# Performance work log

Hardware: AMD Instinct MI355X
Metric: run time of the kernel (lower is better)

## Reference

```python
import jax, jax.numpy as jnp
import numpy as np

B, N, F_IN, DEG = 8, 4096, 8, 8
E = B * N * DEG
MAX_RADIUS, NUM_BASIS, HIDDEN = 3.0, 10, 64
MUL0, MUL1 = 32, 16  # irreps_potential = '32x0e + 16x1o'
W_NUMEL = F_IN * (MUL0 + MUL1)  # 384


def setup_inputs() -> dict:
    key = jax.random.key(0)
    k1, k2, k3, k4, k5, k6 = jax.random.split(key, 6)
    node_features = jax.random.normal(k1, (B, N, F_IN), jnp.float32)
    pos = 4.0 * jax.random.uniform(k2, (B, N, 3), dtype=jnp.float32)  # box so many pairs fall inside max_radius
    # static-shape stand-in for radius_graph: DEG random neighbors per node, within each graph, no self loops
    src = jax.random.randint(k3, (B, N * DEG), 0, N)
    off = jax.random.randint(k4, (B, N * DEG), 1, N)
    dst = (src + off) % N
    boff = (jnp.arange(B) * N)[:, None]
    edge_src = (src + boff).reshape(-1).astype(jnp.int32)
    edge_dst = (dst + boff).reshape(-1).astype(jnp.int32)
    W1 = jax.random.normal(k5, (NUM_BASIS, HIDDEN), jnp.float32)
    W2 = jax.random.normal(k6, (HIDDEN, W_NUMEL), jnp.float32)
    return {"node_features": node_features, "pos": pos, "edge_src": edge_src,
            "edge_dst": edge_dst, "W1": W1, "W2": W2}


def _forward(node_features, pos, edge_src, edge_dst, W1, W2):
    pos_flat = pos.reshape(-1, 3)            # [B*N, 3]
    x_flat = node_features.reshape(-1, F_IN)  # [B*N, F_IN]
    edge_vec = pos_flat[edge_src] - pos_flat[edge_dst]  # [E,3]
    r = jnp.sqrt(jnp.sum(edge_vec * edge_vec, axis=1) + 1e-18)  # [E]

    # soft_one_hot_linspace(r, 0, R, num_basis, basis='smooth_finite', cutoff=True) * sqrt(num_basis)
    values = jnp.linspace(0.0, MAX_RADIUS, NUM_BASIS + 2)[1:-1]
    step = values[1] - values[0]
    d = (r[:, None] - values[None, :]) / step
    inside = jnp.abs(d) < 1.0
    y = jnp.where(inside, jnp.maximum(1.0 - d * d, 1e-7), 1.0)
    emb = jnp.where(inside, 1.14136 * jnp.exp(2.0) * jnp.exp(-1.0 / y), 0.0)
    emb = emb * (NUM_BASIS ** 0.5)           # [E, num_basis]

    # soft_unit_step(10 * (1 - r/R))
    t = 10.0 * (1.0 - r / MAX_RADIUS)
    w_cut = jnp.where(t > 0.0, jnp.exp(-1.0 / jnp.where(t > 0.0, t, 1.0)), 0.0)

    # spherical harmonics lmax=2, normalize=True, 'component' normalization
    u = edge_vec / r[:, None]
    ux, uy, uz = u[:, 0], u[:, 1], u[:, 2]
    sh1 = jnp.sqrt(3.0) * u                  # l=1 (component norm); sh0 == 1
    c15 = np.sqrt(15.0)
    sh2 = jnp.stack([c15 * ux * uy, c15 * uy * uz, 0.5 * np.sqrt(5.0) * (3 * uz * uz - 1.0),
                     c15 * ux * uz, 0.5 * c15 * (ux * ux - uy * uy)], axis=1)
    del sh2  # 2e couples 0e input only to 2e, which is absent from '32x0e+16x1o' -> no path

    # FullyConnectedNet([num_basis, hidden, weight_numel], silu) -> per-edge TP weights
    h = jax.nn.silu(emb @ (W1 / np.sqrt(NUM_BASIS)))
    w = h @ (W2 / np.sqrt(HIDDEN))           # [E, 384]
    wA = w[:, : F_IN * MUL0].reshape(-1, F_IN, MUL0)
    wB = w[:, F_IN * MUL0:].reshape(-1, F_IN, MUL1)

    # FullyConnectedTensorProduct (uvw), shared_weights=False, path norm 1/sqrt(fan_in)
    x_src = x_flat[edge_src]                 # gather [E, F_IN]
    inv = 1.0 / np.sqrt(F_IN)
    out0 = jnp.einsum('eu,euw->ew', x_src, wA) * inv            # 0e x 0e -> 32x0e
    out1 = jnp.einsum('eu,ei,euw->ewi', x_src, sh1, wB) * inv   # 0e x 1o -> 16x1o
    potential = jnp.concatenate([out0, out1.reshape(-1, 3 * MUL1)], axis=1)  # [E, 80]

    # scatter-add to destination nodes
    nodes = jax.ops.segment_sum(w_cut[:, None] * potential, edge_dst, num_segments=B * N)
    psi = nodes[:, :3].reshape(B, N, 3)
    curl = jnp.stack([psi[..., 2] - psi[..., 1],
                      psi[..., 0] - psi[..., 2],
                      psi[..., 1] - psi[..., 0]], axis=-1)       # [B, N, 3]
    return curl


def reference(node_features, pos, edge_src, edge_dst, W1, W2):
    return _forward(node_features, pos, edge_src, edge_dst, W1, W2)
```

## Files before the change

### kernel.cpp

```cpp
#include <hip/hip_runtime.h>
#include <hip/hip_fp16.h>


#define THREADS 256
#define RTAB 2048
#define ROWH 32

__global__ __launch_bounds__(THREADS) void se3_build_table(
    const float* __restrict__ W1,
    const float* __restrict__ W2,
    __half* __restrict__ T,
    float4* __restrict__ zbuf,
    int zcount4)
{
    __shared__ float sW1[10 * 65];
    __shared__ float sW2[64][25];

    for (int t = threadIdx.x; t < 640; t += THREADS) {
        int j = t >> 6, k = t & 63;
        sW1[j * 65 + k] = W1[t];
    }
    for (int t = threadIdx.x; t < 64 * 24; t += THREADS) {
        int k = t / 24, j = t - 24 * k;
        int u = j / 3, c = j - 3 * u;
        sW2[k][j] = W2[k * 384 + u * 32 + c];
    }

    int g = blockIdx.x * THREADS + threadIdx.x;

    float4 z = make_float4(0.f, 0.f, 0.f, 0.f);
    for (int idx = g; idx < zcount4; idx += gridDim.x * THREADS)
        zbuf[idx] = z;

    __syncthreads();

    if (g >= RTAB * 8) return;
    int i = g >> 3;
    int u = g & 7;

    float r = 3.0f * (float)i / (float)(RTAB - 1);
    float q0 = 0.f, q1 = 0.f;
    float t10 = 10.0f - (10.0f / 3.0f) * r;
    if (t10 > 0.0f) {
        const float C0 = 8.43357306907549f;
        float q  = r * (11.0f / 3.0f);
        int   jf = (int)q;
        float da = q - (float)jf;
        float db = da - 1.0f;
        float ya = fmaxf(1.0f - da * da, 1e-7f);
        float yb = fmaxf(1.0f - db * db, 1e-7f);
        int ja = jf - 1, jb = jf;
        float ea = (ja >= 0) ? C0 * __expf(-1.0f / ya) : 0.0f;
        float eb = (jb <= 9) ? C0 * __expf(-1.0f / yb) : 0.0f;
        int jac = ja < 0 ? 0 : ja;
        int jbc = jb > 9 ? 9 : jb;
        const float* w1a = sW1 + jac * 65;
        const float* w1b = sW1 + jbc * 65;

        float a0 = 0.f, a1 = 0.f, a2 = 0.f;
#pragma unroll 8
        for (int k = 0; k < 64; ++k) {
            float pre = ea * w1a[k] + eb * w1b[k];
            float h   = pre * __builtin_amdgcn_rcpf(1.0f + __expf(-pre));
            a0 = fmaf(h, sW2[k][u * 3 + 0], a0);
            a1 = fmaf(h, sW2[k][u * 3 + 1], a1);
            a2 = fmaf(h, sW2[k][u * 3 + 2], a2);
        }
        float sc = __expf(-1.0f / t10) * 0.04419417382415922f;
        q0 = (a2 - a1) * sc;
        q1 = (a0 - a2) * sc;
    }

    __half h0 = __float2half(q0);
    __half h1 = __float2half(q1);
    size_t base = (size_t)i * ROWH + 4 * u;
    T[base + 0] = h0;
    T[base + 2] = h1;
    if (i > 0) {
        T[base - ROWH + 1] = h0;
        T[base - ROWH + 3] = h1;
    }
    if (i == RTAB - 1) {
        T[base + 1] = h0;
        T[base + 3] = h1;
    }
}

__global__ __launch_bounds__(THREADS) void se3_edge_kernel(
    const float* __restrict__ x,
    const float* __restrict__ pos,
    const int*   __restrict__ esrc,
    const int*   __restrict__ edst,
    const __half* __restrict__ T,
    float*       __restrict__ outbuf,
    int E, int ncopies, int outN2)
{
    int e = blockIdx.x * THREADS + threadIdx.x;
    if (e >= E) return;

    int s = esrc[e];
    int d = edst[e];

    float ex = pos[3 * s + 0] - pos[3 * d + 0];
    float ey = pos[3 * s + 1] - pos[3 * d + 1];
    float ez = pos[3 * s + 2] - pos[3 * d + 2];
    float r  = sqrtf(ex * ex + ey * ey + ez * ez + 1e-18f);

    if (r >= 3.0f) return;

    float tq = r * ((float)(RTAB - 1) / 3.0f);
    int   i  = (int)tq;
    if (i > RTAB - 2) i = RTAB - 2;
    float f  = tq - (float)i;

    const float4* rowp = reinterpret_cast<const float4*>(T + (size_t)i * ROWH);
    const float4* xf   = reinterpret_cast<const float4*>(x + 8 * (size_t)s);
    float4 r0 = rowp[0], r1 = rowp[1], r2 = rowp[2], r3 = rowp[3];
    float4 xA = xf[0];
    float4 xB = xf[1];
    float x0 = xA.x, x1 = xA.y, x2 = xA.z, x3 = xA.w;
    float x4 = xB.x, x5 = xB.y, x6 = xB.z, x7 = xB.w;

    float c0 = 0.f, c1 = 0.f;
    auto proc = [&](float4 v, float xu, float xv) {
        union { float4 f4; __half2 h[4]; } cv; cv.f4 = v;
        float2 a0 = __half22float2(cv.h[0]);
        float2 a1 = __half22float2(cv.h[1]);
        float2 a2 = __half22float2(cv.h[2]);
        float2 a3 = __half22float2(cv.h[3]);
        c0 = fmaf(xu, fmaf(f, a0.y - a0.x, a0.x), c0);
        c1 = fmaf(xu, fmaf(f, a1.y - a1.x, a1.x), c1);
        c0 = fmaf(xv, fmaf(f, a2.y - a2.x, a2.x), c0);
        c1 = fmaf(xv, fmaf(f, a3.y - a3.x, a3.x), c1);
    };
    proc(r0, x0, x1);
    proc(r1, x2, x3);
    proc(r2, x4, x5);
    proc(r3, x6, x7);

    float* ob = outbuf + (size_t)(blockIdx.x % ncopies) * outN2 + 2 * d;
    unsafeAtomicAdd(ob + 0, c0);
    unsafeAtomicAdd(ob + 1, c1);
}

__global__ __launch_bounds__(THREADS) void se3_reduce_kernel(
    const float* __restrict__ ws, float* __restrict__ out,
    int nNodes, int ncopies, int outN2)
{
    int n = blockIdx.x * THREADS + threadIdx.x;
    if (n >= nNodes) return;
    const float2* w = reinterpret_cast<const float2*>(ws);
    int stride2 = outN2 >> 1;
    float a = 0.f, b = 0.f;
    for (int c = 0; c < ncopies; ++c) {
        float2 v = w[(size_t)c * stride2 + n];
        a += v.x; b += v.y;
    }
    out[3 * n + 0] = a;
    out[3 * n + 1] = b;
    out[3 * n + 2] = -a - b;
}

extern "C" void kernel_launch(void* const* d_in, const int* in_sizes, int n_in,
                              void* d_out, int out_size, void* d_ws, size_t ws_size,
                              hipStream_t stream) {
    const float* x    = (const float*)d_in[0];
    const float* pos  = (const float*)d_in[1];
    const int*   esrc = (const int*)d_in[2];
    const int*   edst = (const int*)d_in[3];
    const float* W1   = (const float*)d_in[4];
    const float* W2   = (const float*)d_in[5];
    float* out = (float*)d_out;

    int E      = in_sizes[2];
    int outN   = out_size;
    int nNodes = outN / 3;
    int outN2  = 2 * nNodes;

    size_t tableBytes = (size_t)RTAB * ROWH * sizeof(__half);
    __half* T      = (__half*)d_ws;
    float*  copies = (float*)((char*)d_ws + tableBytes);

    size_t copyBytes = (size_t)outN2 * sizeof(float);
    int ncopies = 1;
    if (ws_size > tableBytes + copyBytes) {
        size_t rem = ws_size - tableBytes;
        int nc = (int)(rem / copyBytes);
        if (nc > 8) nc = 8;
        if (nc < 1) nc = 1;
        ncopies = nc;
    }
    int zcount4 = (int)(((size_t)ncopies * outN2) / 4);

    se3_build_table<<<(RTAB * 8) / THREADS, THREADS, 0, stream>>>(
        W1, W2, T, (float4*)copies, zcount4);

    se3_edge_kernel<<<(E + THREADS - 1) / THREADS, THREADS, 0, stream>>>(
        x, pos, esrc, edst, T, copies, E, ncopies, outN2);

    se3_reduce_kernel<<<(nNodes + THREADS - 1) / THREADS, THREADS, 0, stream>>>(
        copies, out, nNodes, ncopies, outN2);
}
```

Baseline: 95.78 us.

## Fuse table build and edge scatter into one cooperative kernel with grid sync

Replaces the three launches (table build with zeroing, edge scatter into replicated buffers, reduction) with a single cooperative kernel. It zeroes the output, builds the lookup table, does a grid-wide sync, then runs a grid-stride edge loop that atomically adds all three curl components straight into the output. The W2 differences are also precomputed in shared memory, so the table loop needs two FMAs per step instead of three. This removes launch overhead and the reduce pass, at the cost of a grid barrier, more atomics per edge (three instead of two) and contention on a single output copy. There are also host-side occupancy queries on every call.

New measurement: 218.0 us. 128% more time.

```diff
diff --git a/kernel.cpp b/kernel.cpp
--- a/kernel.cpp
+++ b/kernel.cpp
@@ -1,40 +1,34 @@
 #include <hip/hip_runtime.h>
 #include <hip/hip_fp16.h>
+#include <hip/hip_cooperative_groups.h>
+
+namespace cg = cooperative_groups;
 
 
 #define THREADS 256
 #define RTAB 2048
 #define ROWH 32
-
-__global__ __launch_bounds__(THREADS) void se3_build_table(
-    const float* __restrict__ W1,
-    const float* __restrict__ W2,
-    __half* __restrict__ T,
-    float4* __restrict__ zbuf,
-    int zcount4)
-{
-    __shared__ float sW1[10 * 65];
-    __shared__ float sW2[64][25];
-
+#define TBLOCKS ((RTAB * 8) / THREADS)
+
+
+__device__ __forceinline__ void stage_weights(const float* __restrict__ W1,
+                                              const float* __restrict__ W2,
+                                              float* sW1, float* sDW2) {
     for (int t = threadIdx.x; t < 640; t += THREADS) {
         int j = t >> 6, k = t & 63;
         sW1[j * 65 + k] = W1[t];
     }
-    for (int t = threadIdx.x; t < 64 * 24; t += THREADS) {
-        int k = t / 24, j = t - 24 * k;
-        int u = j / 3, c = j - 3 * u;
-        sW2[k][j] = W2[k * 384 + u * 32 + c];
-    }
-
-    int g = blockIdx.x * THREADS + threadIdx.x;
-
-    float4 z = make_float4(0.f, 0.f, 0.f, 0.f);
-    for (int idx = g; idx < zcount4; idx += gridDim.x * THREADS)
-        zbuf[idx] = z;
-
-    __syncthreads();
-
-    if (g >= RTAB * 8) return;
+    for (int t = threadIdx.x; t < 64 * 16; t += THREADS) {
+        int k = t >> 4, j = t & 15;
+        int u = j >> 1;
+        const float* w2 = W2 + k * 384 + u * 32;
+        sDW2[t] = (j & 1) ? (w2[0] - w2[2]) : (w2[2] - w2[1]);
+    }
+}
+
+__device__ __forceinline__ void table_entry(int g, const float* sW1,
+                                            const float* sDW2,
+                                            __half* __restrict__ T) {
     int i = g >> 3;
     int u = g & 7;
 
@@ -56,19 +50,19 @@
         int jbc = jb > 9 ? 9 : jb;
         const float* w1a = sW1 + jac * 65;
         const float* w1b = sW1 + jbc * 65;
-
-        float a0 = 0.f, a1 = 0.f, a2 = 0.f;
+        const float* dw  = sDW2 + 2 * u;
+
+        float a0 = 0.f, a1 = 0.f;
 #pragma unroll 8
         for (int k = 0; k < 64; ++k) {
             float pre = ea * w1a[k] + eb * w1b[k];
             float h   = pre * __builtin_amdgcn_rcpf(1.0f + __expf(-pre));
-            a0 = fmaf(h, sW2[k][u * 3 + 0], a0);
-            a1 = fmaf(h, sW2[k][u * 3 + 1], a1);
-            a2 = fmaf(h, sW2[k][u * 3 + 2], a2);
+            a0 = fmaf(h, dw[16 * k + 0], a0);
+            a1 = fmaf(h, dw[16 * k + 1], a1);
         }
         float sc = __expf(-1.0f / t10) * 0.04419417382415922f;
-        q0 = (a2 - a1) * sc;
-        q1 = (a0 - a2) * sc;
+        q0 = a0 * sc;
+        q1 = a1 * sc;
     }
 
     __half h0 = __float2half(q0);
@@ -86,18 +80,11 @@
     }
 }
 
-__global__ __launch_bounds__(THREADS) void se3_edge_kernel(
-    const float* __restrict__ x,
-    const float* __restrict__ pos,
-    const int*   __restrict__ esrc,
-    const int*   __restrict__ edst,
-    const __half* __restrict__ T,
-    float*       __restrict__ outbuf,
-    int E, int ncopies, int outN2)
-{
-    int e = blockIdx.x * THREADS + threadIdx.x;
-    if (e >= E) return;
-
+__device__ __forceinline__ void edge_work(int e,
+    const float* __restrict__ x, const float* __restrict__ pos,
+    const int* __restrict__ esrc, const int* __restrict__ edst,
+    const __half* __restrict__ T, float* __restrict__ out)
+{
     int s = esrc[e];
     int d = edst[e];
 
@@ -118,8 +105,6 @@
     float4 r0 = rowp[0], r1 = rowp[1], r2 = rowp[2], r3 = rowp[3];
     float4 xA = xf[0];
     float4 xB = xf[1];
-    float x0 = xA.x, x1 = xA.y, x2 = xA.z, x3 = xA.w;
-    float x4 = xB.x, x5 = xB.y, x6 = xB.z, x7 = xB.w;
 
     float c0 = 0.f, c1 = 0.f;
     auto proc = [&](float4 v, float xu, float xv) {
@@ -133,33 +118,73 @@
         c0 = fmaf(xv, fmaf(f, a2.y - a2.x, a2.x), c0);
         c1 = fmaf(xv, fmaf(f, a3.y - a3.x, a3.x), c1);
     };
-    proc(r0, x0, x1);
-    proc(r1, x2, x3);
-    proc(r2, x4, x5);
-    proc(r3, x6, x7);
-
-    float* ob = outbuf + (size_t)(blockIdx.x % ncopies) * outN2 + 2 * d;
+    proc(r0, xA.x, xA.y);
+    proc(r1, xA.z, xA.w);
+    proc(r2, xB.x, xB.y);
+    proc(r3, xB.z, xB.w);
+
+    float* ob = out + 3 * (size_t)d;
     unsafeAtomicAdd(ob + 0, c0);
     unsafeAtomicAdd(ob + 1, c1);
-}
-
-__global__ __launch_bounds__(THREADS) void se3_reduce_kernel(
-    const float* __restrict__ ws, float* __restrict__ out,
-    int nNodes, int ncopies, int outN2)
-{
-    int n = blockIdx.x * THREADS + threadIdx.x;
-    if (n >= nNodes) return;
-    const float2* w = reinterpret_cast<const float2*>(ws);
-    int stride2 = outN2 >> 1;
-    float a = 0.f, b = 0.f;
-    for (int c = 0; c < ncopies; ++c) {
-        float2 v = w[(size_t)c * stride2 + n];
-        a += v.x; b += v.y;
-    }
-    out[3 * n + 0] = a;
-    out[3 * n + 1] = b;
-    out[3 * n + 2] = -a - b;
-}
+    unsafeAtomicAdd(ob + 2, -c0 - c1);
+}
+
+
+__global__ __launch_bounds__(THREADS) void se3_fused(
+    const float* __restrict__ x, const float* __restrict__ pos,
+    const int* __restrict__ esrc, const int* __restrict__ edst,
+    const float* __restrict__ W1, const float* __restrict__ W2,
+    __half* __restrict__ T, float* __restrict__ out, int E, int outN)
+{
+    __shared__ float sW1[10 * 65];
+    __shared__ float sDW2[64 * 16];
+
+    int tid = blockIdx.x * THREADS + threadIdx.x;
+    int nth = gridDim.x * THREADS;
+
+    float4 z = make_float4(0.f, 0.f, 0.f, 0.f);
+    for (int idx = tid; idx < (outN >> 2); idx += nth)
+        reinterpret_cast<float4*>(out)[idx] = z;
+
+    if (blockIdx.x < TBLOCKS) {
+        stage_weights(W1, W2, sW1, sDW2);
+        __syncthreads();
+        table_entry(tid, sW1, sDW2, T);
+    }
+
+    cg::this_grid().sync();
+
+    for (int e = tid; e < E; e += nth)
+        edge_work(e, x, pos, esrc, edst, T, out);
+}
+
+
+__global__ __launch_bounds__(THREADS) void se3_build_split(
+    const float* __restrict__ W1, const float* __restrict__ W2,
+    __half* __restrict__ T, float4* __restrict__ zbuf, int zcount4)
+{
+    __shared__ float sW1[10 * 65];
+    __shared__ float sDW2[64 * 16];
+
+    int g = blockIdx.x * THREADS + threadIdx.x;
+    float4 z = make_float4(0.f, 0.f, 0.f, 0.f);
+    for (int idx = g; idx < zcount4; idx += gridDim.x * THREADS)
+        zbuf[idx] = z;
+
+    stage_weights(W1, W2, sW1, sDW2);
+    __syncthreads();
+    if (g < RTAB * 8) table_entry(g, sW1, sDW2, T);
+}
+
+__global__ __launch_bounds__(THREADS) void se3_edge_split(
+    const float* __restrict__ x, const float* __restrict__ pos,
+    const int* __restrict__ esrc, const int* __restrict__ edst,
+    const __half* __restrict__ T, float* __restrict__ out, int E)
+{
+    int e = blockIdx.x * THREADS + threadIdx.x;
+    if (e < E) edge_work(e, x, pos, esrc, edst, T, out);
+}
+
 
 extern "C" void kernel_launch(void* const* d_in, const int* in_sizes, int n_in,
                               void* d_out, int out_size, void* d_ws, size_t ws_size,
@@ -172,32 +197,38 @@
     const float* W2   = (const float*)d_in[5];
     float* out = (float*)d_out;
 
-    int E      = in_sizes[2];
-    int outN   = out_size;
-    int nNodes = outN / 3;
-    int outN2  = 2 * nNodes;
-
-    size_t tableBytes = (size_t)RTAB * ROWH * sizeof(__half);
-    __half* T      = (__half*)d_ws;
-    float*  copies = (float*)((char*)d_ws + tableBytes);
-
-    size_t copyBytes = (size_t)outN2 * sizeof(float);
-    int ncopies = 1;
-    if (ws_size > tableBytes + copyBytes) {
-        size_t rem = ws_size - tableBytes;
-        int nc = (int)(rem / copyBytes);
-        if (nc > 8) nc = 8;
-        if (nc < 1) nc = 1;
-        ncopies = nc;
-    }
-    int zcount4 = (int)(((size_t)ncopies * outN2) / 4);
-
-    se3_build_table<<<(RTAB * 8) / THREADS, THREADS, 0, stream>>>(
-        W1, W2, T, (float4*)copies, zcount4);
-
-    se3_edge_kernel<<<(E + THREADS - 1) / THREADS, THREADS, 0, stream>>>(
-        x, pos, esrc, edst, T, copies, E, ncopies, outN2);
-
-    se3_reduce_kernel<<<(nNodes + THREADS - 1) / THREADS, THREADS, 0, stream>>>(
-        copies, out, nNodes, ncopies, outN2);
-}
+    int E    = in_sizes[2];
+    int outN = out_size;
+    __half* T = (__half*)d_ws;
+
+    int blocksPerCU = 0;
+    if (hipOccupancyMaxActiveBlocksPerMultiprocessor(
+            &blocksPerCU, se3_fused, THREADS, 0) != hipSuccess || blocksPerCU < 1)
+        blocksPerCU = 2;
+    int nCU = 0;
+    int dev = 0;
+    (void)hipGetDevice(&dev);
+    if (hipDeviceGetAttribute(&nCU, hipDeviceAttributeMultiprocessorCount, dev)
+            != hipSuccess || nCU < 1)
+        nCU = 256;
+
+    long cap  = (long)blocksPerCU * (long)nCU;
+    int  grid = (E + THREADS - 1) / THREADS;
+    if ((long)grid > cap) grid = (int)cap;
+    if (grid < TBLOCKS) grid = TBLOCKS;
+
+    void* args[] = {(void*)&x, (void*)&pos, (void*)&esrc, (void*)&edst,
+                    (void*)&W1, (void*)&W2, (void*)&T, (void*)&out,
+                    (void*)&E, (void*)&outN};
+
+    hipError_t err = hipLaunchCooperativeKernel(
+        se3_fused, dim3(grid), dim3(THREADS), args, 0, stream);
+
+    if (err != hipSuccess) {
+        (void)hipGetLastError();
+        se3_build_split<<<TBLOCKS, THREADS, 0, stream>>>(
+            W1, W2, T, (float4*)out, outN / 4);
+        se3_edge_split<<<(E + THREADS - 1) / THREADS, THREADS, 0, stream>>>(
+            x, pos, esrc, edst, T, out, E);
+    }
+}
```

## Repack positions to float4, precompute W2 differences, raise atomic copy count

Applied to the files above, without the earlier changes.

The table-build kernel now also repacks node positions into a padded float4 array so the edge kernel fetches each endpoint with one vector load instead of three scalar gathers. The W2 column differences used for the curl are folded into shared memory ahead of the hidden-unit loop, which cuts one accumulator per thread. The number of atomic-target copies may now go up to sixteen, spreading contention at the cost of more zeroing and reduction traffic, and the build kernel runs on a larger grid to cover the repack and zero passes.

After: 96.48 us. Within noise of the previous version (+0.7%).

```diff
diff --git a/kernel.cpp b/kernel.cpp
--- a/kernel.cpp
+++ b/kernel.cpp
@@ -5,36 +5,48 @@
 #define THREADS 256
 #define RTAB 2048
 #define ROWH 32
+#define TBLOCKS ((RTAB * 8) / THREADS)
+#define BBLOCKS 256
+#define MAXCOPIES 16
 
 __global__ __launch_bounds__(THREADS) void se3_build_table(
     const float* __restrict__ W1,
     const float* __restrict__ W2,
+    const float* __restrict__ pos,
     __half* __restrict__ T,
+    float4* __restrict__ pos4,
     float4* __restrict__ zbuf,
-    int zcount4)
+    int nNodes, int zcount4)
 {
     __shared__ float sW1[10 * 65];
-    __shared__ float sW2[64][25];
+    __shared__ float sDW2[64 * 16];
+
+    int g   = blockIdx.x * THREADS + threadIdx.x;
+    int nth = gridDim.x * THREADS;
+
+    float4 z = make_float4(0.f, 0.f, 0.f, 0.f);
+    for (int idx = g; idx < zcount4; idx += nth)
+        zbuf[idx] = z;
+
+    for (int n = g; n < nNodes; n += nth) {
+        const float* p = pos + 3 * (size_t)n;
+        pos4[n] = make_float4(p[0], p[1], p[2], 0.f);
+    }
+
+    if (blockIdx.x >= TBLOCKS) return;
 
     for (int t = threadIdx.x; t < 640; t += THREADS) {
         int j = t >> 6, k = t & 63;
         sW1[j * 65 + k] = W1[t];
     }
-    for (int t = threadIdx.x; t < 64 * 24; t += THREADS) {
-        int k = t / 24, j = t - 24 * k;
-        int u = j / 3, c = j - 3 * u;
-        sW2[k][j] = W2[k * 384 + u * 32 + c];
-    }
-
-    int g = blockIdx.x * THREADS + threadIdx.x;
-
-    float4 z = make_float4(0.f, 0.f, 0.f, 0.f);
-    for (int idx = g; idx < zcount4; idx += gridDim.x * THREADS)
-        zbuf[idx] = z;
-
+    for (int t = threadIdx.x; t < 64 * 16; t += THREADS) {
+        int k = t >> 4, j = t & 15;
+        int u = j >> 1;
+        const float* w2 = W2 + k * 384 + u * 32;
+        sDW2[t] = (j & 1) ? (w2[0] - w2[2]) : (w2[2] - w2[1]);
+    }
     __syncthreads();
 
-    if (g >= RTAB * 8) return;
     int i = g >> 3;
     int u = g & 7;
 
@@ -56,19 +68,19 @@
         int jbc = jb > 9 ? 9 : jb;
         const float* w1a = sW1 + jac * 65;
         const float* w1b = sW1 + jbc * 65;
-
-        float a0 = 0.f, a1 = 0.f, a2 = 0.f;
+        const float* dw  = sDW2 + 2 * u;
+
+        float a0 = 0.f, a1 = 0.f;
 #pragma unroll 8
         for (int k = 0; k < 64; ++k) {
             float pre = ea * w1a[k] + eb * w1b[k];
             float h   = pre * __builtin_amdgcn_rcpf(1.0f + __expf(-pre));
-            a0 = fmaf(h, sW2[k][u * 3 + 0], a0);
-            a1 = fmaf(h, sW2[k][u * 3 + 1], a1);
-            a2 = fmaf(h, sW2[k][u * 3 + 2], a2);
+            a0 = fmaf(h, dw[16 * k + 0], a0);
+            a1 = fmaf(h, dw[16 * k + 1], a1);
         }
         float sc = __expf(-1.0f / t10) * 0.04419417382415922f;
-        q0 = (a2 - a1) * sc;
-        q1 = (a0 - a2) * sc;
+        q0 = a0 * sc;
+        q1 = a1 * sc;
     }
 
     __half h0 = __float2half(q0);
@@ -87,12 +99,12 @@
 }
 
 __global__ __launch_bounds__(THREADS) void se3_edge_kernel(
-    const float* __restrict__ x,
-    const float* __restrict__ pos,
-    const int*   __restrict__ esrc,
-    const int*   __restrict__ edst,
+    const float*  __restrict__ x,
+    const float4* __restrict__ pos4,
+    const int*    __restrict__ esrc,
+    const int*    __restrict__ edst,
     const __half* __restrict__ T,
-    float*       __restrict__ outbuf,
+    float*        __restrict__ outbuf,
     int E, int ncopies, int outN2)
 {
     int e = blockIdx.x * THREADS + threadIdx.x;
@@ -101,9 +113,11 @@
     int s = esrc[e];
     int d = edst[e];
 
-    float ex = pos[3 * s + 0] - pos[3 * d + 0];
-    float ey = pos[3 * s + 1] - pos[3 * d + 1];
-    float ez = pos[3 * s + 2] - pos[3 * d + 2];
+    float4 ps = pos4[s];
+    float4 pd = pos4[d];
+    float ex = ps.x - pd.x;
+    float ey = ps.y - pd.y;
+    float ez = ps.z - pd.z;
     float r  = sqrtf(ex * ex + ey * ey + ez * ez + 1e-18f);
 
     if (r >= 3.0f) return;
@@ -118,8 +132,6 @@
     float4 r0 = rowp[0], r1 = rowp[1], r2 = rowp[2], r3 = rowp[3];
     float4 xA = xf[0];
     float4 xB = xf[1];
-    float x0 = xA.x, x1 = xA.y, x2 = xA.z, x3 = xA.w;
-    float x4 = xB.x, x5 = xB.y, x6 = xB.z, x7 = xB.w;
 
     float c0 = 0.f, c1 = 0.f;
     auto proc = [&](float4 v, float xu, float xv) {
@@ -133,10 +145,10 @@
         c0 = fmaf(xv, fmaf(f, a2.y - a2.x, a2.x), c0);
         c1 = fmaf(xv, fmaf(f, a3.y - a3.x, a3.x), c1);
     };
-    proc(r0, x0, x1);
-    proc(r1, x2, x3);
-    proc(r2, x4, x5);
-    proc(r3, x6, x7);
+    proc(r0, xA.x, xA.y);
+    proc(r1, xA.z, xA.w);
+    proc(r2, xB.x, xB.y);
+    proc(r3, xB.z, xB.w);
 
     float* ob = outbuf + (size_t)(blockIdx.x % ncopies) * outN2 + 2 * d;
     unsafeAtomicAdd(ob + 0, c0);
@@ -156,9 +168,9 @@
         float2 v = w[(size_t)c * stride2 + n];
         a += v.x; b += v.y;
     }
-    out[3 * n + 0] = a;
-    out[3 * n + 1] = b;
-    out[3 * n + 2] = -a - b;
+    out[3 * (size_t)n + 0] = a;
+    out[3 * (size_t)n + 1] = b;
+    out[3 * (size_t)n + 2] = -a - b;
 }
 
 extern "C" void kernel_launch(void* const* d_in, const int* in_sizes, int n_in,
@@ -178,25 +190,27 @@
     int outN2  = 2 * nNodes;
 
     size_t tableBytes = (size_t)RTAB * ROWH * sizeof(__half);
+    size_t pos4Bytes  = (size_t)nNodes * sizeof(float4);
     __half* T      = (__half*)d_ws;
-    float*  copies = (float*)((char*)d_ws + tableBytes);
+    float4* pos4   = (float4*)((char*)d_ws + tableBytes);
+    float*  copies = (float*)((char*)d_ws + tableBytes + pos4Bytes);
 
     size_t copyBytes = (size_t)outN2 * sizeof(float);
     int ncopies = 1;
-    if (ws_size > tableBytes + copyBytes) {
-        size_t rem = ws_size - tableBytes;
+    if (ws_size > tableBytes + pos4Bytes + copyBytes) {
+        size_t rem = ws_size - tableBytes - pos4Bytes;
         int nc = (int)(rem / copyBytes);
-        if (nc > 8) nc = 8;
+        if (nc > MAXCOPIES) nc = MAXCOPIES;
         if (nc < 1) nc = 1;
         ncopies = nc;
     }
     int zcount4 = (int)(((size_t)ncopies * outN2) / 4);
 
-    se3_build_table<<<(RTAB * 8) / THREADS, THREADS, 0, stream>>>(
-        W1, W2, T, (float4*)copies, zcount4);
+    se3_build_table<<<BBLOCKS, THREADS, 0, stream>>>(
+        W1, W2, pos, T, pos4, (float4*)copies, nNodes, zcount4);
 
     se3_edge_kernel<<<(E + THREADS - 1) / THREADS, THREADS, 0, stream>>>(
-        x, pos, esrc, edst, T, copies, E, ncopies, outN2);
+        x, pos4, esrc, edst, T, copies, E, ncopies, outN2);
 
     se3_reduce_kernel<<<(nNodes + THREADS - 1) / THREADS, THREADS, 0, stream>>>(
         copies, out, nNodes, ncopies, outN2);
```
